# Optimization experiments

Measured on AMD Instinct MI355X. Metric: run time of the kernel, lower is better.

## Reference

```python
import jax, jax.numpy as jnp
import numpy as np

N_NODES = 8192
N_EDGES = 262144
D_IN = 512
D_OUT = 512


def setup_inputs() -> dict:
    key = jax.random.key(0)
    k1, k2, k3 = jax.random.split(key, 3)
    x = jax.random.normal(k1, (N_NODES, D_IN), dtype=jnp.float32)
    edge_index = jax.random.randint(k2, (2, N_EDGES), 0, N_NODES, dtype=jnp.int64)
    weight = jax.random.normal(k3, (D_IN, D_OUT), dtype=jnp.float32)
    bias = jnp.zeros((D_OUT,), dtype=jnp.float32)
    return {"x": x, "edge_index": edge_index, "weight": weight, "bias": bias}


def reference(x, edge_index, weight, bias):
    # GCN layer with selfloop=True branch of the original module.
    n = x.shape[0]
    # Dense symmetric adjacency via scatter-set, matching adj[ei0,ei1]=1; adj[ei1,ei0]=1
    adj = jnp.zeros((n, n), dtype=x.dtype)
    adj = adj.at[edge_index[0], edge_index[1]].set(1.0)
    adj = adj.at[edge_index[1], edge_index[0]].set(1.0)
    # Add self loops, symmetric degree normalization D^{-1/2} A D^{-1/2}
    adj = adj + jnp.eye(n, dtype=x.dtype)
    deg = jnp.sum(adj, axis=1)
    dinv = 1.0 / jnp.sqrt(deg)
    adj = adj * dinv[:, None] * dinv[None, :]  # == D @ adj @ D (diagonal scaling)
    return adj @ (x @ weight) + bias
```

## Files before the change

### kernel.cpp

```cpp
#include <hip/hip_runtime.h>
#include <hip/hip_bf16.h>


#define ELL_STRIDE 128

typedef __attribute__((ext_vector_type(8))) short bf16x8;
typedef __attribute__((ext_vector_type(4))) float f32x4;

__device__ __forceinline__ unsigned short f2bf(float f) {
  unsigned u = __float_as_uint(f);
  u = (u + 0x7fff + ((u >> 16) & 1)) >> 16;
  return (unsigned short)u;
}
__device__ __forceinline__ float bflo(unsigned u) {
  return __uint_as_float(u << 16);
}
__device__ __forceinline__ float bfhi(unsigned u) {
  return __uint_as_float(u & 0xffff0000u);
}

__global__ __launch_bounds__(256) void fused_front_kernel(
    const int* __restrict__ ei, unsigned* __restrict__ mask, int n_edges,
    int words,
    const float* __restrict__ x, unsigned short* __restrict__ xb, int n4,
    const float* __restrict__ W, unsigned short* __restrict__ Wt, int K, int N,
    unsigned short* __restrict__ Hs, float* __restrict__ dinv, int n_nodes,
    int edge_blocks, int cast_blocks, int tr_blocks) {
  const int bid = blockIdx.x;
  if (bid < edge_blocks) {
    const int e = bid * 256 + threadIdx.x;
    if (e < n_edges) {
      const int u = ei[e];
      const int v = ei[e + n_edges];
      atomicOr(&mask[(size_t)u * words + (v >> 5)], 1u << (v & 31));
      atomicOr(&mask[(size_t)v * words + (u >> 5)], 1u << (u & 31));
    }
    return;
  }
  if (bid < edge_blocks + cast_blocks) {
    const int t = (bid - edge_blocks) * 256 + threadIdx.x;
    if (t < n4) {
      float4 v = ((const float4*)x)[t];
      ushort4 o;
      o.x = f2bf(v.x); o.y = f2bf(v.y); o.z = f2bf(v.z); o.w = f2bf(v.w);
      ((ushort4*)xb)[t] = o;
    }
    return;
  }
  if (bid < edge_blocks + cast_blocks + tr_blocks) {
    __shared__ float tile[32][33];
    const int b = bid - edge_blocks - cast_blocks;
    const int bx = b & ((N >> 5) - 1);
    const int by = b >> (31 - __builtin_clz(N >> 5));
    const int tx = threadIdx.x & 31;
    const int ty = threadIdx.x >> 5;
#pragma unroll
    for (int r = 0; r < 4; ++r)
      tile[ty + 8 * r][tx] = W[(size_t)(by * 32 + ty + 8 * r) * N + bx * 32 + tx];
    __syncthreads();
#pragma unroll
    for (int r = 0; r < 4; ++r)
      Wt[(size_t)(bx * 32 + ty + 8 * r) * K + by * 32 + tx] =
          f2bf(tile[tx][ty + 8 * r]);
    return;
  }
  {
    const int t = threadIdx.x;
    if (t < (N >> 1)) ((unsigned*)(Hs + (size_t)n_nodes * N))[t] = 0;
    if (t == 0) dinv[n_nodes] = 0.f;
  }
}

__global__ __launch_bounds__(256) void fused_mid_kernel(
    const unsigned short* __restrict__ xb,
    const unsigned short* __restrict__ Wt,
    unsigned short* __restrict__ Hs,
    const unsigned* __restrict__ mask, unsigned short* __restrict__ ell,
    int* __restrict__ deg, float* __restrict__ dinv,
    int M, int N, int K, int words, int gemm_blocks, int nbx_sh) {
  __shared__ unsigned short As[1024 * 8];
  __shared__ unsigned short Bs[1024 * 8];

  const int tid = threadIdx.x;
  const int bid = blockIdx.x;

  if (bid < gemm_blocks) {
    const int wave = tid >> 6;
    const int lane = tid & 63;
    const int q = lane >> 4;
    const int c = lane & 15;
    const int bx = bid & ((1 << nbx_sh) - 1);
    const int by = bid >> nbx_sh;
    const int m0 = by * 128;
    const int n0 = bx * 128;
    const int wr = wave >> 1, wc = wave & 1;

    f32x4 acc[4][4] = {};

    for (int k0 = 0; k0 < K; k0 += 64) {
#pragma unroll
      for (int t = 0; t < 4; ++t) {
        const int sbase = t * 256 + wave * 64;
        const int s = sbase + lane;
        const unsigned short* g =
            xb + (size_t)(m0 + (s & 127)) * K + k0 + (s >> 7) * 8;
        __builtin_amdgcn_global_load_lds(
            (const __attribute__((address_space(1))) void*)g,
            (__attribute__((address_space(3))) void*)(As + sbase * 8), 16, 0, 0);
      }
#pragma unroll
      for (int t = 0; t < 4; ++t) {
        const int sbase = t * 256 + wave * 64;
        const int s = sbase + lane;
        const int bn = s >> 3;
        const int bk = (s & 7) ^ (bn & 7);
        const unsigned short* g =
            Wt + (size_t)(n0 + bn) * K + k0 + bk * 8;
        __builtin_amdgcn_global_load_lds(
            (const __attribute__((address_space(1))) void*)g,
            (__attribute__((address_space(3))) void*)(Bs + sbase * 8), 16, 0, 0);
      }
      __syncthreads();

#pragma unroll
      for (int kk = 0; kk < 2; ++kk) {
        bf16x8 a[4], b[4];
#pragma unroll
        for (int tm = 0; tm < 4; ++tm) {
          const int row = wr * 64 + tm * 16 + c;
          a[tm] = *(const bf16x8*)(As + (((kk * 4 + q) * 128) + row) * 8);
        }
#pragma unroll
        for (int tn = 0; tn < 4; ++tn) {
          const int n = wc * 64 + tn * 16 + c;
          b[tn] = *(const bf16x8*)(Bs + (n * 8 + ((kk * 4 + q) ^ (n & 7))) * 8);
        }
#pragma unroll
        for (int tm = 0; tm < 4; ++tm)
#pragma unroll
          for (int tn = 0; tn < 4; ++tn)
            acc[tm][tn] = __builtin_amdgcn_mfma_f32_16x16x32_bf16(
                a[tm], b[tn], acc[tm][tn], 0, 0, 0);
      }
      __syncthreads();
    }

#pragma unroll
    for (int tm = 0; tm < 4; ++tm) {
#pragma unroll
      for (int r = 0; r < 4; ++r) {
        const int grow = m0 + wr * 64 + tm * 16 + q * 4 + r;
#pragma unroll
        for (int tn = 0; tn < 4; ++tn) {
          const int gcol = n0 + wc * 64 + tn * 16 + c;
          Hs[(size_t)grow * N + gcol] = f2bf(acc[tm][tn][r]);
        }
      }
    }
    return;
  }

  {
    const int wave = tid >> 6, lane = tid & 63;
    const int node = (bid - gemm_blocks) * 4 + wave;
    const unsigned* __restrict__ row = mask + (size_t)node * words;
    unsigned short* __restrict__ out = ell + (size_t)node * ELL_STRIDE;

    int running = 0;
    for (int r = 0; r < words; r += 64) {
      const int w = r + lane;
      unsigned bits = row[w];
      const int cnt = __popc(bits);
      int x = cnt;
#pragma unroll
      for (int d = 1; d < 64; d <<= 1) {
        int y = __shfl_up(x, d, 64);
        if (lane >= d) x += y;
      }
      int pos = running + x - cnt;
      while (bits) {
        const int b = __builtin_ctz(bits);
        bits &= bits - 1;
        if (pos < ELL_STRIDE) out[pos] = (unsigned short)((w << 5) + b);
        ++pos;
      }
      running += __shfl(x, 63, 64);
    }
    for (int p = running + lane; p < ELL_STRIDE; p += 64)
      out[p] = (unsigned short)(p == running ? node : M);
    if (lane == 0) {
      const int dd = running + 1;
      deg[node] = dd < ELL_STRIDE ? dd : ELL_STRIDE;
      dinv[node] = rsqrtf((float)running + 1.0f);
    }
  }
}

__global__ __launch_bounds__(256) void spmm_kernel(
    const unsigned short* __restrict__ ell, const int* __restrict__ deg,
    const float* __restrict__ dinv, const unsigned short* __restrict__ Hs,
    const float* __restrict__ bias, float* __restrict__ out, int n, int D) {
  __shared__ uint2 ji[4][ELL_STRIDE];
  const int wave = threadIdx.x >> 6, lane = threadIdx.x & 63;
  const int i = blockIdx.x * 4 + wave;
  const unsigned rowbytes = (unsigned)(D * 2);

  {
    const unsigned j0 =
        __builtin_nontemporal_load(ell + (size_t)i * ELL_STRIDE + lane);
    const unsigned j1 =
        __builtin_nontemporal_load(ell + (size_t)i * ELL_STRIDE + 64 + lane);
    ji[wave][lane] = make_uint2(j0 * rowbytes, __float_as_uint(dinv[j0]));
    ji[wave][64 + lane] = make_uint2(j1 * rowbytes, __float_as_uint(dinv[j1]));
  }
  const int d = deg[i];
  const float di = dinv[i];
  const int kmax = (d + 15) & ~15;

  const char* __restrict__ hb = (const char*)(Hs + lane * 8);
  float acc[8] = {0.f, 0.f, 0.f, 0.f, 0.f, 0.f, 0.f, 0.f};

#pragma unroll 16
  for (int k = 0; k < kmax; ++k) {
    const uint2 e = ji[wave][k];
    const float dj = __uint_as_float(e.y);
    const uint4 hv = *(const uint4*)(hb + e.x);
    acc[0] += dj * bflo(hv.x); acc[1] += dj * bfhi(hv.x);
    acc[2] += dj * bflo(hv.y); acc[3] += dj * bfhi(hv.y);
    acc[4] += dj * bflo(hv.z); acc[5] += dj * bfhi(hv.z);
    acc[6] += dj * bflo(hv.w); acc[7] += dj * bfhi(hv.w);
  }

  const float4 b0 = *(const float4*)(bias + lane * 8);
  const float4 b1 = *(const float4*)(bias + lane * 8 + 4);
  float* op = out + (size_t)i * D + lane * 8;
  f32x4 o0, o1;
  o0.x = di * acc[0] + b0.x; o0.y = di * acc[1] + b0.y;
  o0.z = di * acc[2] + b0.z; o0.w = di * acc[3] + b0.w;
  o1.x = di * acc[4] + b1.x; o1.y = di * acc[5] + b1.y;
  o1.z = di * acc[6] + b1.z; o1.w = di * acc[7] + b1.w;
  __builtin_nontemporal_store(o0, (f32x4*)op);
  __builtin_nontemporal_store(o1, (f32x4*)(op + 4));
}

extern "C" void kernel_launch(void* const* d_in, const int* in_sizes, int n_in,
                              void* d_out, int out_size, void* d_ws, size_t ws_size,
                              hipStream_t stream) {
  const float* x    = (const float*)d_in[0];
  const int*   ei   = (const int*)d_in[1];
  const float* W    = (const float*)d_in[2];
  const float* bias = (const float*)d_in[3];
  float* out = (float*)d_out;

  const int d_out_dim = in_sizes[3];
  const int d_in_dim  = in_sizes[2] / d_out_dim;
  const int n_nodes   = in_sizes[0] / d_in_dim;
  const int n_edges   = in_sizes[1] / 2;
  const int words     = (n_nodes + 31) / 32;

  char* ws = (char*)d_ws;
  size_t off = 0;
  unsigned* mask = (unsigned*)(ws + off); off += (size_t)n_nodes * words * 4;
  int* deg       = (int*)(ws + off);      off += (size_t)n_nodes * 4;
  float* dinv    = (float*)(ws + off);    off += (size_t)(n_nodes + 1) * 4;
  unsigned short* ell = (unsigned short*)(ws + off); off += (size_t)n_nodes * ELL_STRIDE * 2;
  unsigned short* xb  = (unsigned short*)(ws + off); off += (size_t)n_nodes * d_in_dim * 2;
  unsigned short* Wt  = (unsigned short*)(ws + off); off += (size_t)d_in_dim * d_out_dim * 2;
  unsigned short* Hs  = (unsigned short*)(ws + off);
  off += (size_t)(n_nodes + 1) * d_out_dim * 2;

  hipMemsetAsync(mask, 0, (size_t)n_nodes * words * 4, stream);

  const int edge_blocks = (n_edges + 255) / 256;
  const int n4 = n_nodes * d_in_dim / 4;
  const int cast_blocks = (n4 + 255) / 256;
  const int tr_blocks = (d_in_dim / 32) * (d_out_dim / 32);
  fused_front_kernel<<<edge_blocks + cast_blocks + tr_blocks + 1, 256, 0, stream>>>(
      ei, mask, n_edges, words, x, xb, n4, W, Wt, d_in_dim, d_out_dim,
      Hs, dinv, n_nodes, edge_blocks, cast_blocks, tr_blocks);

  const int nbx = d_out_dim / 128;
  const int nbx_sh = 31 - __builtin_clz(nbx);
  const int gemm_blocks = nbx * (n_nodes / 128);
  const int ell_blocks = n_nodes / 4;
  fused_mid_kernel<<<gemm_blocks + ell_blocks, 256, 0, stream>>>(
      xb, Wt, Hs, mask, ell, deg, dinv,
      n_nodes, d_out_dim, d_in_dim, words, gemm_blocks, nbx_sh);

  spmm_kernel<<<n_nodes / 4, 256, 0, stream>>>(ell, deg, dinv, Hs, bias, out,
                                               n_nodes, d_out_dim);
}
```

Measured before the change: 160.2 us.

## Build ELL adjacency in LDS per node block and software-pipeline SpMM gathers

Drops the global 8 MB bitmask, its memset and the global atomics. Each block of 64 nodes now scans the whole edge list and builds its rows' bitmask in shared memory, then compacts it straight into ELL form. The GEMM becomes a standalone kernel, split out of the old fused GEMM/ELL kernel. The SpMM loop now prefetches 8 neighbor rows ahead into registers, using padding entries that point at a zero row. The cost is that every block rereads the full edge list, and the adjacency kernel launches only n/64 blocks of 512 threads, which may underfill the GPU.

Result: slower. 206.0 us (+28.6%).

```diff
diff --git a/kernel.cpp b/kernel.cpp
--- a/kernel.cpp
+++ b/kernel.cpp
@@ -19,26 +19,91 @@
   return __uint_as_float(u & 0xffff0000u);
 }
 
-__global__ __launch_bounds__(256) void fused_front_kernel(
-    const int* __restrict__ ei, unsigned* __restrict__ mask, int n_edges,
-    int words,
+__global__ __launch_bounds__(512) void adj_ell_kernel(
+    const int* __restrict__ ei, unsigned short* __restrict__ ell,
+    int* __restrict__ deg, float* __restrict__ dinv,
+    int n_nodes, int n_edges, int words) {
+  __shared__ unsigned sm[64 * 256];
+
+  const int tid = threadIdx.x;
+  const int base = blockIdx.x << 6;
+
+#pragma unroll
+  for (int t = tid; t < 64 * 256; t += 512) sm[t] = 0u;
+  __syncthreads();
+
+  {
+    const int4* __restrict__ eu4 = (const int4*)ei;
+    const int4* __restrict__ ev4 = (const int4*)(ei + n_edges);
+    const int nq = n_edges >> 2;
+    for (int t = tid; t < nq; t += 512) {
+      const int4 u4 = eu4[t];
+      const int4 v4 = ev4[t];
+#define PROC(uu, vv)                                                        \
+  {                                                                         \
+    const int u_ = (uu), v_ = (vv);                                         \
+    if ((unsigned)(u_ - base) < 64u)                                        \
+      atomicOr(&sm[((u_ - base) << 8) + (v_ >> 5)], 1u << (v_ & 31));       \
+    if ((unsigned)(v_ - base) < 64u)                                        \
+      atomicOr(&sm[((v_ - base) << 8) + (u_ >> 5)], 1u << (u_ & 31));       \
+  }
+      PROC(u4.x, v4.x) PROC(u4.y, v4.y) PROC(u4.z, v4.z) PROC(u4.w, v4.w)
+#undef PROC
+    }
+  }
+  __syncthreads();
+
+  {
+    const int wave = tid >> 6, lane = tid & 63;
+    for (int s = 0; s < 8; ++s) {
+      const int nl = wave * 8 + s;
+      const int node = base + nl;
+      unsigned w[4];
+      int cnt = 0;
+#pragma unroll
+      for (int j = 0; j < 4; ++j) {
+        w[j] = sm[(nl << 8) + lane + j * 64];
+        cnt += __popc(w[j]);
+      }
+      int x = cnt;
+#pragma unroll
+      for (int d = 1; d < 64; d <<= 1) {
+        int y = __shfl_up(x, d, 64);
+        if (lane >= d) x += y;
+      }
+      int pos = x - cnt;
+      const int total = __shfl(x, 63, 64);
+      unsigned short* __restrict__ out = ell + (size_t)node * ELL_STRIDE;
+#pragma unroll
+      for (int j = 0; j < 4; ++j) {
+        unsigned bits = w[j];
+        const int wj = lane + j * 64;
+        while (bits) {
+          const int b = __builtin_ctz(bits);
+          bits &= bits - 1;
+          if (pos < ELL_STRIDE) out[pos] = (unsigned short)((wj << 5) + b);
+          ++pos;
+        }
+      }
+      for (int p = total + lane; p < ELL_STRIDE; p += 64)
+        out[p] = (unsigned short)(p == total ? node : n_nodes);
+      if (lane == 0) {
+        const int dd = total + 1;
+        deg[node] = dd < ELL_STRIDE ? dd : ELL_STRIDE;
+        dinv[node] = rsqrtf((float)total + 1.0f);
+      }
+    }
+  }
+}
+
+__global__ __launch_bounds__(256) void prep_kernel(
     const float* __restrict__ x, unsigned short* __restrict__ xb, int n4,
     const float* __restrict__ W, unsigned short* __restrict__ Wt, int K, int N,
     unsigned short* __restrict__ Hs, float* __restrict__ dinv, int n_nodes,
-    int edge_blocks, int cast_blocks, int tr_blocks) {
+    int cast_blocks, int tr_blocks) {
   const int bid = blockIdx.x;
-  if (bid < edge_blocks) {
-    const int e = bid * 256 + threadIdx.x;
-    if (e < n_edges) {
-      const int u = ei[e];
-      const int v = ei[e + n_edges];
-      atomicOr(&mask[(size_t)u * words + (v >> 5)], 1u << (v & 31));
-      atomicOr(&mask[(size_t)v * words + (u >> 5)], 1u << (u & 31));
-    }
-    return;
-  }
-  if (bid < edge_blocks + cast_blocks) {
-    const int t = (bid - edge_blocks) * 256 + threadIdx.x;
+  if (bid < cast_blocks) {
+    const int t = bid * 256 + threadIdx.x;
     if (t < n4) {
       float4 v = ((const float4*)x)[t];
       ushort4 o;
@@ -47,9 +112,9 @@
     }
     return;
   }
-  if (bid < edge_blocks + cast_blocks + tr_blocks) {
+  if (bid < cast_blocks + tr_blocks) {
     __shared__ float tile[32][33];
-    const int b = bid - edge_blocks - cast_blocks;
+    const int b = bid - cast_blocks;
     const int bx = b & ((N >> 5) - 1);
     const int by = b >> (31 - __builtin_clz(N >> 5));
     const int tx = threadIdx.x & 31;
@@ -71,127 +136,86 @@
   }
 }
 
-__global__ __launch_bounds__(256) void fused_mid_kernel(
+__global__ __launch_bounds__(256) void gemm_kernel(
     const unsigned short* __restrict__ xb,
     const unsigned short* __restrict__ Wt,
     unsigned short* __restrict__ Hs,
-    const unsigned* __restrict__ mask, unsigned short* __restrict__ ell,
-    int* __restrict__ deg, float* __restrict__ dinv,
-    int M, int N, int K, int words, int gemm_blocks, int nbx_sh) {
+    int M, int N, int K, int nbx_sh) {
   __shared__ unsigned short As[1024 * 8];
   __shared__ unsigned short Bs[1024 * 8];
 
   const int tid = threadIdx.x;
   const int bid = blockIdx.x;
-
-  if (bid < gemm_blocks) {
-    const int wave = tid >> 6;
-    const int lane = tid & 63;
-    const int q = lane >> 4;
-    const int c = lane & 15;
-    const int bx = bid & ((1 << nbx_sh) - 1);
-    const int by = bid >> nbx_sh;
-    const int m0 = by * 128;
-    const int n0 = bx * 128;
-    const int wr = wave >> 1, wc = wave & 1;
-
-    f32x4 acc[4][4] = {};
-
-    for (int k0 = 0; k0 < K; k0 += 64) {
-#pragma unroll
-      for (int t = 0; t < 4; ++t) {
-        const int sbase = t * 256 + wave * 64;
-        const int s = sbase + lane;
-        const unsigned short* g =
-            xb + (size_t)(m0 + (s & 127)) * K + k0 + (s >> 7) * 8;
-        __builtin_amdgcn_global_load_lds(
-            (const __attribute__((address_space(1))) void*)g,
-            (__attribute__((address_space(3))) void*)(As + sbase * 8), 16, 0, 0);
-      }
-#pragma unroll
-      for (int t = 0; t < 4; ++t) {
-        const int sbase = t * 256 + wave * 64;
-        const int s = sbase + lane;
-        const int bn = s >> 3;
-        const int bk = (s & 7) ^ (bn & 7);
-        const unsigned short* g =
-            Wt + (size_t)(n0 + bn) * K + k0 + bk * 8;
-        __builtin_amdgcn_global_load_lds(
-            (const __attribute__((address_space(1))) void*)g,
-            (__attribute__((address_space(3))) void*)(Bs + sbase * 8), 16, 0, 0);
-      }
-      __syncthreads();
-
-#pragma unroll
-      for (int kk = 0; kk < 2; ++kk) {
-        bf16x8 a[4], b[4];
-#pragma unroll
-        for (int tm = 0; tm < 4; ++tm) {
-          const int row = wr * 64 + tm * 16 + c;
-          a[tm] = *(const bf16x8*)(As + (((kk * 4 + q) * 128) + row) * 8);
-        }
-#pragma unroll
-        for (int tn = 0; tn < 4; ++tn) {
-          const int n = wc * 64 + tn * 16 + c;
-          b[tn] = *(const bf16x8*)(Bs + (n * 8 + ((kk * 4 + q) ^ (n & 7))) * 8);
-        }
-#pragma unroll
-        for (int tm = 0; tm < 4; ++tm)
-#pragma unroll
-          for (int tn = 0; tn < 4; ++tn)
-            acc[tm][tn] = __builtin_amdgcn_mfma_f32_16x16x32_bf16(
-                a[tm], b[tn], acc[tm][tn], 0, 0, 0);
-      }
-      __syncthreads();
-    }
-
-#pragma unroll
-    for (int tm = 0; tm < 4; ++tm) {
-#pragma unroll
-      for (int r = 0; r < 4; ++r) {
-        const int grow = m0 + wr * 64 + tm * 16 + q * 4 + r;
-#pragma unroll
-        for (int tn = 0; tn < 4; ++tn) {
-          const int gcol = n0 + wc * 64 + tn * 16 + c;
-          Hs[(size_t)grow * N + gcol] = f2bf(acc[tm][tn][r]);
-        }
-      }
-    }
-    return;
-  }
-
-  {
-    const int wave = tid >> 6, lane = tid & 63;
-    const int node = (bid - gemm_blocks) * 4 + wave;
-    const unsigned* __restrict__ row = mask + (size_t)node * words;
-    unsigned short* __restrict__ out = ell + (size_t)node * ELL_STRIDE;
-
-    int running = 0;
-    for (int r = 0; r < words; r += 64) {
-      const int w = r + lane;
-      unsigned bits = row[w];
-      const int cnt = __popc(bits);
-      int x = cnt;
-#pragma unroll
-      for (int d = 1; d < 64; d <<= 1) {
-        int y = __shfl_up(x, d, 64);
-        if (lane >= d) x += y;
-      }
-      int pos = running + x - cnt;
-      while (bits) {
-        const int b = __builtin_ctz(bits);
-        bits &= bits - 1;
-        if (pos < ELL_STRIDE) out[pos] = (unsigned short)((w << 5) + b);
-        ++pos;
-      }
-      running += __shfl(x, 63, 64);
-    }
-    for (int p = running + lane; p < ELL_STRIDE; p += 64)
-      out[p] = (unsigned short)(p == running ? node : M);
-    if (lane == 0) {
-      const int dd = running + 1;
-      deg[node] = dd < ELL_STRIDE ? dd : ELL_STRIDE;
-      dinv[node] = rsqrtf((float)running + 1.0f);
+  const int wave = tid >> 6;
+  const int lane = tid & 63;
+  const int q = lane >> 4;
+  const int c = lane & 15;
+  const int bx = bid & ((1 << nbx_sh) - 1);
+  const int by = bid >> nbx_sh;
+  const int m0 = by * 128;
+  const int n0 = bx * 128;
+  const int wr = wave >> 1, wc = wave & 1;
+
+  f32x4 acc[4][4] = {};
+
+  for (int k0 = 0; k0 < K; k0 += 64) {
+#pragma unroll
+    for (int t = 0; t < 4; ++t) {
+      const int sbase = t * 256 + wave * 64;
+      const int s = sbase + lane;
+      const unsigned short* g =
+          xb + (size_t)(m0 + (s & 127)) * K + k0 + (s >> 7) * 8;
+      __builtin_amdgcn_global_load_lds(
+          (const __attribute__((address_space(1))) void*)g,
+          (__attribute__((address_space(3))) void*)(As + sbase * 8), 16, 0, 0);
+    }
+#pragma unroll
+    for (int t = 0; t < 4; ++t) {
+      const int sbase = t * 256 + wave * 64;
+      const int s = sbase + lane;
+      const int bn = s >> 3;
+      const int bk = (s & 7) ^ (bn & 7);
+      const unsigned short* g =
+          Wt + (size_t)(n0 + bn) * K + k0 + bk * 8;
+      __builtin_amdgcn_global_load_lds(
+          (const __attribute__((address_space(1))) void*)g,
+          (__attribute__((address_space(3))) void*)(Bs + sbase * 8), 16, 0, 0);
+    }
+    __syncthreads();
+
+#pragma unroll
+    for (int kk = 0; kk < 2; ++kk) {
+      bf16x8 a[4], b[4];
+#pragma unroll
+      for (int tm = 0; tm < 4; ++tm) {
+        const int row = wr * 64 + tm * 16 + c;
+        a[tm] = *(const bf16x8*)(As + (((kk * 4 + q) * 128) + row) * 8);
+      }
+#pragma unroll
+      for (int tn = 0; tn < 4; ++tn) {
+        const int n = wc * 64 + tn * 16 + c;
+        b[tn] = *(const bf16x8*)(Bs + (n * 8 + ((kk * 4 + q) ^ (n & 7))) * 8);
+      }
+#pragma unroll
+      for (int tm = 0; tm < 4; ++tm)
+#pragma unroll
+        for (int tn = 0; tn < 4; ++tn)
+          acc[tm][tn] = __builtin_amdgcn_mfma_f32_16x16x32_bf16(
+              a[tm], b[tn], acc[tm][tn], 0, 0, 0);
+    }
+    __syncthreads();
+  }
+
+#pragma unroll
+  for (int tm = 0; tm < 4; ++tm) {
+#pragma unroll
+    for (int r = 0; r < 4; ++r) {
+      const int grow = m0 + wr * 64 + tm * 16 + q * 4 + r;
+#pragma unroll
+      for (int tn = 0; tn < 4; ++tn) {
+        const int gcol = n0 + wc * 64 + tn * 16 + c;
+        Hs[(size_t)grow * N + gcol] = f2bf(acc[tm][tn][r]);
+      }
     }
   }
 }
@@ -200,35 +224,47 @@
     const unsigned short* __restrict__ ell, const int* __restrict__ deg,
     const float* __restrict__ dinv, const unsigned short* __restrict__ Hs,
     const float* __restrict__ bias, float* __restrict__ out, int n, int D) {
-  __shared__ uint2 ji[4][ELL_STRIDE];
+  __shared__ uint2 ji[4][ELL_STRIDE + 8];
   const int wave = threadIdx.x >> 6, lane = threadIdx.x & 63;
   const int i = blockIdx.x * 4 + wave;
   const unsigned rowbytes = (unsigned)(D * 2);
 
   {
-    const unsigned j0 =
-        __builtin_nontemporal_load(ell + (size_t)i * ELL_STRIDE + lane);
-    const unsigned j1 =
-        __builtin_nontemporal_load(ell + (size_t)i * ELL_STRIDE + 64 + lane);
+    const unsigned j0 = ell[(size_t)i * ELL_STRIDE + lane];
+    const unsigned j1 = ell[(size_t)i * ELL_STRIDE + 64 + lane];
     ji[wave][lane] = make_uint2(j0 * rowbytes, __float_as_uint(dinv[j0]));
     ji[wave][64 + lane] = make_uint2(j1 * rowbytes, __float_as_uint(dinv[j1]));
+    if (lane < 8)
+      ji[wave][ELL_STRIDE + lane] = make_uint2((unsigned)n * rowbytes, 0u);
   }
   const int d = deg[i];
   const float di = dinv[i];
-  const int kmax = (d + 15) & ~15;
+  const int kmax = (d + 7) & ~7;
 
   const char* __restrict__ hb = (const char*)(Hs + lane * 8);
   float acc[8] = {0.f, 0.f, 0.f, 0.f, 0.f, 0.f, 0.f, 0.f};
 
-#pragma unroll 16
-  for (int k = 0; k < kmax; ++k) {
-    const uint2 e = ji[wave][k];
-    const float dj = __uint_as_float(e.y);
-    const uint4 hv = *(const uint4*)(hb + e.x);
-    acc[0] += dj * bflo(hv.x); acc[1] += dj * bfhi(hv.x);
-    acc[2] += dj * bflo(hv.y); acc[3] += dj * bfhi(hv.y);
-    acc[4] += dj * bflo(hv.z); acc[5] += dj * bfhi(hv.z);
-    acc[6] += dj * bflo(hv.w); acc[7] += dj * bfhi(hv.w);
+  uint4 pf[8];
+  unsigned dj[8];
+#pragma unroll
+  for (int p = 0; p < 8; ++p) {
+    const uint2 e = ji[wave][p];
+    dj[p] = e.y;
+    pf[p] = *(const uint4*)(hb + e.x);
+  }
+  for (int k = 0; k < kmax; k += 8) {
+#pragma unroll
+    for (int p = 0; p < 8; ++p) {
+      const float djv = __uint_as_float(dj[p]);
+      const uint4 hv = pf[p];
+      acc[0] += djv * bflo(hv.x); acc[1] += djv * bfhi(hv.x);
+      acc[2] += djv * bflo(hv.y); acc[3] += djv * bfhi(hv.y);
+      acc[4] += djv * bflo(hv.z); acc[5] += djv * bfhi(hv.z);
+      acc[6] += djv * bflo(hv.w); acc[7] += djv * bfhi(hv.w);
+      const uint2 e = ji[wave][k + 8 + p];
+      dj[p] = e.y;
+      pf[p] = *(const uint4*)(hb + e.x);
+    }
   }
 
   const float4 b0 = *(const float4*)(bias + lane * 8);
@@ -260,7 +296,6 @@
 
   char* ws = (char*)d_ws;
   size_t off = 0;
-  unsigned* mask = (unsigned*)(ws + off); off += (size_t)n_nodes * words * 4;
   int* deg       = (int*)(ws + off);      off += (size_t)n_nodes * 4;
   float* dinv    = (float*)(ws + off);    off += (size_t)(n_nodes + 1) * 4;
   unsigned short* ell = (unsigned short*)(ws + off); off += (size_t)n_nodes * ELL_STRIDE * 2;
@@ -269,23 +304,20 @@
   unsigned short* Hs  = (unsigned short*)(ws + off);
   off += (size_t)(n_nodes + 1) * d_out_dim * 2;
 
-  hipMemsetAsync(mask, 0, (size_t)n_nodes * words * 4, stream);
-
-  const int edge_blocks = (n_edges + 255) / 256;
+  adj_ell_kernel<<<n_nodes / 64, 512, 0, stream>>>(ei, ell, deg, dinv,
+                                                   n_nodes, n_edges, words);
+
   const int n4 = n_nodes * d_in_dim / 4;
   const int cast_blocks = (n4 + 255) / 256;
   const int tr_blocks = (d_in_dim / 32) * (d_out_dim / 32);
-  fused_front_kernel<<<edge_blocks + cast_blocks + tr_blocks + 1, 256, 0, stream>>>(
-      ei, mask, n_edges, words, x, xb, n4, W, Wt, d_in_dim, d_out_dim,
-      Hs, dinv, n_nodes, edge_blocks, cast_blocks, tr_blocks);
+  prep_kernel<<<cast_blocks + tr_blocks + 1, 256, 0, stream>>>(
+      x, xb, n4, W, Wt, d_in_dim, d_out_dim, Hs, dinv, n_nodes,
+      cast_blocks, tr_blocks);
 
   const int nbx = d_out_dim / 128;
   const int nbx_sh = 31 - __builtin_clz(nbx);
-  const int gemm_blocks = nbx * (n_nodes / 128);
-  const int ell_blocks = n_nodes / 4;
-  fused_mid_kernel<<<gemm_blocks + ell_blocks, 256, 0, stream>>>(
-      xb, Wt, Hs, mask, ell, deg, dinv,
-      n_nodes, d_out_dim, d_in_dim, words, gemm_blocks, nbx_sh);
+  gemm_kernel<<<nbx * (n_nodes / 128), 256, 0, stream>>>(
+      xb, Wt, Hs, n_nodes, d_out_dim, d_in_dim, nbx_sh);
 
   spmm_kernel<<<n_nodes / 4, 256, 0, stream>>>(ell, deg, dinv, Hs, bias, out,
                                                n_nodes, d_out_dim);
```
